# Performance work log

Measured on AMD Instinct MI355X. Metric: run time of the kernel, lower is better.

Reference implementation:

```python
import jax, jax.numpy as jnp
import numpy as np

N_P, N_W, F_IN = 512, 3584, 256
H1, O1 = 8, 32
H2, O2 = 8, 256
BATCH = 1024
NEG_SLOPE = 0.2


def _xavier(key, shape):
    fan_in, fan_out = shape[-2], shape[-1]
    lim = jnp.sqrt(6.0 / (fan_in + fan_out))
    return jax.random.uniform(key, shape, jnp.float32, -lim, lim)


def setup_inputs() -> dict:
    key = jax.random.key(0)
    ks = jax.random.split(key, 16)
    return {
        "input": jax.random.uniform(ks[0], (BATCH, N_W), jnp.float32),
        "pern_feature": jax.random.normal(ks[1], (N_P, F_IN), jnp.float32),
        "word_feature": jax.random.normal(ks[2], (N_W, F_IN), jnp.float32),
        "w1": _xavier(ks[3], (H1, F_IN, O1)),
        "a_src1": _xavier(ks[4], (H1, O1, 1)),
        "a_dst1": _xavier(ks[5], (H1, O1, 1)),
        "b1": jnp.zeros((O1,), jnp.float32),
        "w2": _xavier(ks[6], (H2, F_IN, O2)),
        "a_src2": _xavier(ks[7], (H2, F_IN, 1)),
        "a_dst2": _xavier(ks[8], (H2, F_IN, 1)),
        "b2": jnp.zeros((O2,), jnp.float32),
        "W_fc": _xavier(ks[9], (O2, 5)),
        "b_fc": jnp.zeros((5,), jnp.float32),
        "pern_adj": jax.random.randint(ks[10], (N_P, N_P), 0, 2, jnp.int32),
        "word_pern_adj": jax.random.randint(ks[11], (N_P + N_W, N_P + N_W), 0, 2, jnp.int32),
    }


def gat(h, adj, w, a_src, a_dst, bias):
    # h: [N, f_in], adj: [N, N] int, w: [H, f_in, f_out]
    h_prime = jnp.einsum('nf,hfo->hno', h, w)          # [H, N, O]
    t = jnp.tanh(h_prime)
    s_src = jnp.einsum('hno,hoi->hn', t, a_src)        # [H, N]
    s_dst = jnp.einsum('hno,hoi->hn', t, a_dst)        # [H, N]
    attn = s_src[:, :, None] + s_dst[:, None, :]       # [H, N, N]
    attn = jnp.where(attn >= 0, attn, NEG_SLOPE * attn)  # leaky_relu
    attn = jnp.where(adj[None, :, :] > 0, attn, -jnp.inf)
    attn = jax.nn.softmax(attn, axis=-1)
    out = jnp.einsum('hnm,hmo->hno', attn, h_prime)    # [H, N, O]
    return out + bias


def reference(input, pern_feature, word_feature, w1, a_src1, a_dst1, b1,
              w2, a_src2, a_dst2, b2, W_fc, b_fc, pern_adj, word_pern_adj):
    n_p = pern_feature.shape[0]
    # GAT 1 over personality graph
    h1 = gat(pern_feature, pern_adj, w1, a_src1, a_dst1, b1)       # [H1, n_p, O1]
    hiddn_pp = jnp.transpose(h1, (1, 0, 2)).reshape(n_p, -1)        # [n_p, H1*O1]
    hiddn_pp = jax.nn.elu(hiddn_pp)
    # dropout is identity in eval mode
    hiddn_wp = jnp.concatenate([word_feature, hiddn_pp], axis=0)    # [N, 256]
    h2 = gat(hiddn_wp, word_pern_adj, w2, a_src2, a_dst2, b2)       # [H2, N, O2]
    hiddn_wp2 = h2.mean(axis=0)                                     # [N, O2]
    hiddn_w = hiddn_wp2[:word_feature.shape[0], :]                  # [n_w, O2]
    x = (input @ hiddn_w) / input.sum(axis=1, keepdims=True)        # [B, O2]
    return x @ W_fc + b_fc                                          # [B, 5]
```

## Files before the change

### kernel.cpp

```cpp
#include <hip/hip_runtime.h>
#include <hip/hip_bf16.h>
#include <math.h>

#define NP 512
#define NW 3584
#define NT 4096
#define FIN 256
#define H1 8
#define O1 32
#define H2 8
#define O2 256
#define NEG 0.2f

typedef __attribute__((ext_vector_type(8))) short bf16x8;
typedef __attribute__((ext_vector_type(4))) float f32x4;
typedef unsigned long long u64;

__device__ __forceinline__ unsigned short f2bf(float f) {
    unsigned u = __float_as_uint(f);
    unsigned r = (u + 0x7FFF + ((u >> 16) & 1)) >> 16;
    return (unsigned short)r;
}

__device__ __forceinline__ float fast_tanh(float x) {
    float ex = __expf(2.0f * x);
    return 1.0f - 2.0f / (ex + 1.0f);
}

__device__ __forceinline__ float rfl(float x) {
    return __uint_as_float(__builtin_amdgcn_readfirstlane(__float_as_uint(x)));
}

__global__ void k_conv_word(const float* __restrict__ wf, unsigned short* __restrict__ abf) {
    int i = blockIdx.x * 256 + threadIdx.x;
    if (i < NW * FIN) abf[i] = f2bf(wf[i]);
}

__global__ __launch_bounds__(256) void k_gat1_hp(
    const float* __restrict__ pf, const float* __restrict__ w1,
    const float* __restrict__ a_src1, const float* __restrict__ a_dst1,
    float* __restrict__ hp1, float* __restrict__ ss1, float* __restrict__ sd1)
{
    __shared__ float feat[8][FIN];
    int t = threadIdx.x;
    int n0 = blockIdx.x * 8;
    for (int q = 0; q < 8; q++) {
        int idx = q * 256 + t;
        feat[idx >> 8][idx & 255] = pf[(n0 + (idx >> 8)) * FIN + (idx & 255)];
    }
    __syncthreads();
    int h = t >> 5, o = t & 31;
    float acc[8] = {0,0,0,0,0,0,0,0};
    const float* wcol = w1 + h * FIN * O1 + o;
    for (int f = 0; f < FIN; f++) {
        float w = wcol[f * O1];
        #pragma unroll
        for (int i = 0; i < 8; i++) acc[i] += feat[i][f] * w;
    }
    float as = a_src1[h * O1 + o];
    float ad = a_dst1[h * O1 + o];
    #pragma unroll
    for (int i = 0; i < 8; i++) {
        hp1[(n0 + i) * 256 + t] = acc[i];
        float th = tanhf(acc[i]);
        float vs = th * as, vd = th * ad;
        #pragma unroll
        for (int off = 1; off < 32; off <<= 1) {
            vs += __shfl_xor(vs, off);
            vd += __shfl_xor(vd, off);
        }
        if (o == 0) { ss1[h * NP + n0 + i] = vs; sd1[h * NP + n0 + i] = vd; }
    }
}

__global__ __launch_bounds__(256) void k_gat1_attn(
    const int* __restrict__ adj, const float* __restrict__ hp1,
    const float* __restrict__ ss1, const float* __restrict__ sd1,
    const float* __restrict__ b1, unsigned short* __restrict__ abf)
{
    __shared__ float p[2][H1][NP];
    __shared__ float den[2][H1];
    int t = threadIdx.x;
    int n0 = blockIdx.x * 2;
    for (int rr = 0; rr < 32; rr++) {
        int idx = rr * 256 + t;
        int i = idx >> 12, h = (idx >> 9) & 7, m = idx & 511;
        float a = adj[(n0 + i) * NP + m] > 0 ? 1.0f : 0.0f;
        float e = ss1[h * NP + n0 + i] + sd1[h * NP + m];
        e = fmaxf(e, NEG * e);
        p[i][h][m] = a * __expf(e);
    }
    __syncthreads();
    int w = t >> 6, l = t & 63;
    {
        int i = w & 1;
        #pragma unroll
        for (int hh = 0; hh < 4; hh++) {
            int h = (w >> 1) * 4 + hh;
            float s = 0;
            #pragma unroll
            for (int q = 0; q < 8; q++) s += p[i][h][l + 64 * q];
            #pragma unroll
            for (int off = 1; off < 64; off <<= 1) s += __shfl_xor(s, off);
            if (l == 0) den[i][h] = s;
        }
    }
    __syncthreads();
    int h = t >> 5, o = t & 31;
    float acc[2] = {0, 0};
    #pragma unroll 4
    for (int m = 0; m < NP; m++) {
        float v = hp1[m * 256 + t];
        acc[0] += p[0][h][m] * v;
        acc[1] += p[1][h][m] * v;
    }
    float bo = b1[o];
    #pragma unroll
    for (int i = 0; i < 2; i++) {
        float r = acc[i] / den[i][h] + bo;
        r = r > 0.f ? r : expm1f(r);
        abf[(NW + n0 + i) * FIN + t] = f2bf(r);
    }
}

__global__ void k_conv_w2(const float* __restrict__ w2, unsigned short* __restrict__ btbf) {
    int idx = blockIdx.x * 256 + threadIdx.x;
    int f = idx & 255, o = (idx >> 8) & 255, h = idx >> 16;
    btbf[idx] = f2bf(w2[(h * FIN + f) * O2 + o]);
}

__global__ __launch_bounds__(256) void k_pack_adj(const int* __restrict__ adj,
                                                  u64* __restrict__ packed) {
    int w = threadIdx.x >> 6, l = threadIdx.x & 63;
    int r = blockIdx.x * 4 + w;
    const int4* row = (const int4*)(adj + (size_t)r * NT);
    for (int c4 = 0; c4 < 16; c4++) {
        int4 x = row[c4 * 64 + l];
        u64 nib = (u64)((x.x != 0 ? 1 : 0) | (x.y != 0 ? 2 : 0) |
                        (x.z != 0 ? 4 : 0) | (x.w != 0 ? 8 : 0));
        u64 v = nib << (4 * (l & 15));
        v |= __shfl_xor(v, 1);
        v |= __shfl_xor(v, 2);
        v |= __shfl_xor(v, 4);
        v |= __shfl_xor(v, 8);
        if ((l & 15) == 0) packed[(size_t)r * 64 + c4 * 4 + (l >> 4)] = v;
    }
}

__global__ __launch_bounds__(256) void k_gemm_hp2(
    const unsigned short* __restrict__ abf, const unsigned short* __restrict__ btbf,
    const float* __restrict__ a_src2, const float* __restrict__ a_dst2,
    const float* __restrict__ W_fc, float* __restrict__ gpart)
{
    int bid = blockIdx.x;
    int h = bid >> 6;
    int rem = bid & 63;
    int mt = rem >> 1, nt = rem & 1;
    int w = threadIdx.x >> 6, l = threadIdx.x & 63;
    int m0 = mt * 128 + (w >> 1) * 64;
    int n0 = nt * 128 + (w & 1) * 64;
    int lr = l & 15, lq = l >> 4;
    const unsigned short* bbase = btbf + h * O2 * FIN;
    f32x4 acc[4][4];
    #pragma unroll
    for (int i = 0; i < 4; i++)
        #pragma unroll
        for (int j = 0; j < 4; j++) acc[i][j] = (f32x4){0.f, 0.f, 0.f, 0.f};
    for (int k = 0; k < FIN; k += 32) {
        bf16x8 a[4], b[4];
        int kc = k + lq * 8;
        #pragma unroll
        for (int i = 0; i < 4; i++)
            a[i] = *(const bf16x8*)(abf + (m0 + i * 16 + lr) * FIN + kc);
        #pragma unroll
        for (int j = 0; j < 4; j++)
            b[j] = *(const bf16x8*)(bbase + (n0 + j * 16 + lr) * FIN + kc);
        #pragma unroll
        for (int i = 0; i < 4; i++)
            #pragma unroll
            for (int j = 0; j < 4; j++)
                acc[i][j] = __builtin_amdgcn_mfma_f32_16x16x32_bf16(a[i], b[j], acc[i][j], 0, 0, 0);
    }
    int slice = nt * 2 + (w & 1);
    float as[4], ad[4], wfc[4][5];
    #pragma unroll
    for (int j = 0; j < 4; j++) {
        int col = n0 + j * 16 + lr;
        as[j] = a_src2[h * O2 + col];
        ad[j] = a_dst2[h * O2 + col];
        #pragma unroll
        for (int jj = 0; jj < 5; jj++) wfc[j][jj] = W_fc[col * 5 + jj];
    }
    float* base = gpart + ((size_t)h * 4 + slice) * NT * 8;
    #pragma unroll
    for (int i = 0; i < 4; i++) {
        #pragma unroll
        for (int r = 0; r < 4; r++) {
            float s[7] = {0,0,0,0,0,0,0};
            #pragma unroll
            for (int j = 0; j < 4; j++) {
                float x = acc[i][j][r];
                float th = fast_tanh(x);
                s[0] += th * as[j];
                s[1] += th * ad[j];
                #pragma unroll
                for (int jj = 0; jj < 5; jj++) s[2 + jj] += x * wfc[j][jj];
            }
            #pragma unroll
            for (int off = 1; off < 16; off <<= 1)
                #pragma unroll
                for (int q = 0; q < 7; q++) s[q] += __shfl_xor(s[q], off);
            if (lr == 0) {
                int m = m0 + i * 16 + lq * 4 + r;
                float* dst = base + (size_t)m * 8;
                #pragma unroll
                for (int q = 0; q < 7; q++) dst[q] = s[q];
            }
        }
    }
}

__global__ __launch_bounds__(256) void k_comb_hp2(
    const float* __restrict__ gpart,
    float* __restrict__ negss, float* __restrict__ Etab, float* __restrict__ Eptab,
    float* __restrict__ T)
{
    int idx = blockIdx.x * 256 + threadIdx.x;
    float s[7] = {0,0,0,0,0,0,0};
    #pragma unroll
    for (int sl = 0; sl < 4; sl++) {
        const float* p = gpart + (((size_t)(idx >> 12) * 4 + sl) * NT + (idx & (NT - 1))) * 8;
        #pragma unroll
        for (int q = 0; q < 7; q++) s[q] += p[q];
    }
    negss[idx] = -s[0];
    Etab[idx]  = __expf(s[0]);
    Eptab[idx] = __expf(NEG * s[0]);
    float4 t0 = {s[1], __expf(s[1]), __expf(NEG * s[1]), s[2]};
    float4 t1 = {s[3], s[4], s[5], s[6]};
    *(float4*)(T + (size_t)idx * 8)     = t0;
    *(float4*)(T + (size_t)idx * 8 + 4) = t1;
}

__global__ void k_cvec(const float* __restrict__ b2, const float* __restrict__ W_fc,
                       float* __restrict__ c) {
    int t = threadIdx.x;
    float v[5];
    #pragma unroll
    for (int j = 0; j < 5; j++) v[j] = b2[t] * W_fc[t * 5 + j];
    #pragma unroll
    for (int off = 1; off < 64; off <<= 1)
        #pragma unroll
        for (int j = 0; j < 5; j++) v[j] += __shfl_xor(v[j], off);
    __shared__ float red[4][5];
    int w = t >> 6, l = t & 63;
    if (l == 0) { for (int j = 0; j < 5; j++) red[w][j] = v[j]; }
    __syncthreads();
    if (t == 0)
        for (int j = 0; j < 5; j++) c[j] = red[0][j] + red[1][j] + red[2][j] + red[3][j];
}

__global__ __launch_bounds__(512) void k_gat2_attn(
    const u64* __restrict__ packed, const float* __restrict__ negss,
    const float* __restrict__ Etab, const float* __restrict__ Eptab,
    const float* __restrict__ T, float* __restrict__ part)
{
    __shared__ u64 pw[64 * 32];
    int t = threadIdx.x;
    int w = t >> 6, l = t & 63;
    int b = blockIdx.x;
    int nb = b % 56;
    int h  = (b / 56) & 7;
    int c  = b / 448;
    int rbase = nb * 64;
    #pragma unroll
    for (int u = 0; u < 4; u++) {
        int idx = u * 512 + t;
        int row = idx >> 5, q = idx & 31;
        pw[idx] = packed[(size_t)(rbase + row) * 64 + c * 32 + q];
    }
    __syncthreads();
    int n0 = rbase + w * 8;
    float ns[8], E[8], Ep[8];
    #pragma unroll
    for (int i = 0; i < 8; i++) {
        int r = h * NT + n0 + i;
        ns[i] = rfl(negss[r]);
        E[i]  = rfl(Etab[r]);
        Ep[i] = rfl(Eptab[r]);
    }
    float den[8] = {0,0,0,0,0,0,0,0};
    float num[8][5] = {{0}};
    const float* Th = T + ((size_t)h * NT + c * 2048) * 8;
    for (int q = 0; q < 32; q++) {
        const float* tp = Th + (size_t)(q * 64 + l) * 8;
        float4 t0 = *(const float4*)tp;
        float4 t1 = *(const float4*)(tp + 4);
        float sd = t0.x, F = t0.y, Fp = t0.z;
        float g0 = t0.w, g1 = t1.x, g2 = t1.y, g3 = t1.z, g4 = t1.w;
        #pragma unroll
        for (int i = 0; i < 8; i++) {
            u64 word = pw[(w * 8 + i) * 32 + q];
            float pa = F * E[i];
            float pb = Fp * Ep[i];
            float pp0 = (sd >= ns[i]) ? pa : pb;
            float pp = ((word >> l) & 1ull) ? pp0 : 0.0f;
            den[i] += pp;
            num[i][0] = fmaf(pp, g0, num[i][0]);
            num[i][1] = fmaf(pp, g1, num[i][1]);
            num[i][2] = fmaf(pp, g2, num[i][2]);
            num[i][3] = fmaf(pp, g3, num[i][3]);
            num[i][4] = fmaf(pp, g4, num[i][4]);
        }
    }
    #pragma unroll
    for (int i = 0; i < 8; i++) {
        float v[6];
        v[0] = den[i];
        #pragma unroll
        for (int j = 0; j < 5; j++) v[1 + j] = num[i][j];
        #pragma unroll
        for (int off = 1; off < 64; off <<= 1)
            #pragma unroll
            for (int k = 0; k < 6; k++) v[k] += __shfl_xor(v[k], off);
        if (l == 0) {
            float* dst = part + (((size_t)c * NW + n0 + i) * 8 + h) * 6;
            #pragma unroll
            for (int k = 0; k < 6; k++) dst[k] = v[k];
        }
    }
}

__global__ __launch_bounds__(256) void k_gat2_comb(const float* __restrict__ part,
                                                   float* __restrict__ hf) {
    int idx = blockIdx.x * 256 + threadIdx.x;
    int n = idx >> 3, h = idx & 7;
    float den = 0, num[5] = {0,0,0,0,0};
    #pragma unroll
    for (int cc = 0; cc < 2; cc++) {
        const float* p = part + (((size_t)cc * NW + n) * 8 + h) * 6;
        den += p[0];
        #pragma unroll
        for (int j = 0; j < 5; j++) num[j] += p[1 + j];
    }
    float inv = 1.0f / (den * 8.0f);
    float v[5];
    #pragma unroll
    for (int j = 0; j < 5; j++) v[j] = num[j] * inv;
    #pragma unroll
    for (int off = 1; off < 8; off <<= 1)
        #pragma unroll
        for (int j = 0; j < 5; j++) v[j] += __shfl_xor(v[j], off);
    if (h == 0) {
        #pragma unroll
        for (int j = 0; j < 5; j++) hf[n * 5 + j] = v[j];
    }
}

__global__ __launch_bounds__(256) void k_final(
    const float* __restrict__ input, const float* __restrict__ hf,
    const float* __restrict__ cvec, const float* __restrict__ b_fc,
    float* __restrict__ out)
{
    int b = blockIdx.x, t = threadIdx.x;
    const float4* row4 = (const float4*)(input + (size_t)b * NW);
    const float4* hf4 = (const float4*)hf;
    float s = 0.f, a[5] = {0.f, 0.f, 0.f, 0.f, 0.f};
    for (int idx = t; idx < NW / 4; idx += 256) {
        float4 x = row4[idx];
        float f[20];
        #pragma unroll
        for (int q = 0; q < 5; q++) *(float4*)(f + 4 * q) = hf4[idx * 5 + q];
        s += x.x + x.y + x.z + x.w;
        #pragma unroll
        for (int j = 0; j < 5; j++)
            a[j] += x.x * f[j] + x.y * f[5 + j] + x.z * f[10 + j] + x.w * f[15 + j];
    }
    #pragma unroll
    for (int off = 1; off < 64; off <<= 1) {
        s += __shfl_xor(s, off);
        #pragma unroll
        for (int j = 0; j < 5; j++) a[j] += __shfl_xor(a[j], off);
    }
    __shared__ float red[4][6];
    int w = t >> 6, l = t & 63;
    if (l == 0) { red[w][0] = s; for (int j = 0; j < 5; j++) red[w][j + 1] = a[j]; }
    __syncthreads();
    if (t < 5) {
        float st = red[0][0] + red[1][0] + red[2][0] + red[3][0];
        float aj = red[0][t + 1] + red[1][t + 1] + red[2][t + 1] + red[3][t + 1];
        out[b * 5 + t] = aj / st + cvec[t] + b_fc[t];
    }
}

extern "C" void kernel_launch(void* const* d_in, const int* in_sizes, int n_in,
                              void* d_out, int out_size, void* d_ws, size_t ws_size,
                              hipStream_t stream) {
    const float* input   = (const float*)d_in[0];
    const float* pf      = (const float*)d_in[1];
    const float* wf      = (const float*)d_in[2];
    const float* w1      = (const float*)d_in[3];
    const float* a_src1  = (const float*)d_in[4];
    const float* a_dst1  = (const float*)d_in[5];
    const float* b1      = (const float*)d_in[6];
    const float* w2      = (const float*)d_in[7];
    const float* a_src2  = (const float*)d_in[8];
    const float* a_dst2  = (const float*)d_in[9];
    const float* b2      = (const float*)d_in[10];
    const float* W_fc    = (const float*)d_in[11];
    const float* b_fc    = (const float*)d_in[12];
    const int* pern_adj  = (const int*)d_in[13];
    const int* wp_adj    = (const int*)d_in[14];
    float* out = (float*)d_out;

    char* ws = (char*)d_ws;
    unsigned short* abf    = (unsigned short*)(ws);
    unsigned short* btbf   = (unsigned short*)(ws + 2097152);
    float*          hp1    = (float*)(ws + 3145728);
    float*          ss1    = (float*)(ws + 3670016);
    float*          sd1    = (float*)(ws + 3686400);
    float*          negss  = (float*)(ws + 3702784);
    float*          Etab   = (float*)(ws + 3833856);
    float*          Eptab  = (float*)(ws + 3964928);
    float*          T      = (float*)(ws + 4096000);
    float*          hf     = (float*)(ws + 5144576);
    float*          cvec   = (float*)(ws + 5216256);
    u64*            packed = (u64*)(ws + 5216512);
    float*          gpart  = (float*)(ws + 7051520);
    float*          part   = (float*)(ws + 11245824);

    k_conv_word<<<3584, 256, 0, stream>>>(wf, abf);
    k_gat1_hp<<<64, 256, 0, stream>>>(pf, w1, a_src1, a_dst1, hp1, ss1, sd1);
    k_gat1_attn<<<256, 256, 0, stream>>>(pern_adj, hp1, ss1, sd1, b1, abf);
    k_conv_w2<<<2048, 256, 0, stream>>>(w2, btbf);
    k_pack_adj<<<896, 256, 0, stream>>>(wp_adj, packed);
    k_gemm_hp2<<<512, 256, 0, stream>>>(abf, btbf, a_src2, a_dst2, W_fc, gpart);
    k_comb_hp2<<<128, 256, 0, stream>>>(gpart, negss, Etab, Eptab, T);
    k_cvec<<<1, 256, 0, stream>>>(b2, W_fc, cvec);
    k_gat2_attn<<<896, 512, 0, stream>>>(packed, negss, Etab, Eptab, T, part);
    k_gat2_comb<<<112, 256, 0, stream>>>(part, hf);
    k_final<<<1024, 256, 0, stream>>>(input, hf, cvec, b_fc, out);
}
```

Baseline: 297.4 us.

## Merge prep kernels and use packed-math max trick in GAT2 attention loop

Five small preprocessing kernels (word conversion, GAT1 projection, w2 conversion, adjacency packing, bias vector) are merged into one launch with block-range dispatch. The GAT2 attention inner loop drops the sign comparison: since exp is monotonic, the leaky-relu branch equals the max of exp(s) and exp(0.2*s), so the branch becomes v_pk_mul plus fmax. The loop also uses packed FP32 FMAs and reads adjacency words directly from global via readfirstlane instead of staging them in LDS. This cuts launch overhead and ALU work, but relies on inline asm and uncached scalar-broadcast global loads.

New measurement: 314.0 us. 5.6% more time.

```diff
diff --git a/kernel.cpp b/kernel.cpp
--- a/kernel.cpp
+++ b/kernel.cpp
@@ -14,6 +14,7 @@
 
 typedef __attribute__((ext_vector_type(8))) short bf16x8;
 typedef __attribute__((ext_vector_type(4))) float f32x4;
+typedef __attribute__((ext_vector_type(2))) float v2f;
 typedef unsigned long long u64;
 
 __device__ __forceinline__ unsigned short f2bf(float f) {
@@ -27,49 +28,85 @@
     return 1.0f - 2.0f / (ex + 1.0f);
 }
 
-__device__ __forceinline__ float rfl(float x) {
-    return __uint_as_float(__builtin_amdgcn_readfirstlane(__float_as_uint(x)));
-}
-
-__global__ void k_conv_word(const float* __restrict__ wf, unsigned short* __restrict__ abf) {
-    int i = blockIdx.x * 256 + threadIdx.x;
-    if (i < NW * FIN) abf[i] = f2bf(wf[i]);
-}
-
-__global__ __launch_bounds__(256) void k_gat1_hp(
-    const float* __restrict__ pf, const float* __restrict__ w1,
-    const float* __restrict__ a_src1, const float* __restrict__ a_dst1,
-    float* __restrict__ hp1, float* __restrict__ ss1, float* __restrict__ sd1)
-{
-    __shared__ float feat[8][FIN];
+__global__ __launch_bounds__(256) void k_prep(
+    const float* __restrict__ wf, const float* __restrict__ pf,
+    const float* __restrict__ w1, const float* __restrict__ a_src1,
+    const float* __restrict__ a_dst1, const float* __restrict__ w2,
+    const float* __restrict__ b2, const float* __restrict__ W_fc,
+    const int* __restrict__ wp_adj,
+    unsigned short* __restrict__ abf, unsigned short* __restrict__ btbf,
+    float* __restrict__ hp1, float* __restrict__ ss1, float* __restrict__ sd1,
+    u64* __restrict__ packed, float* __restrict__ cvec)
+{
+    __shared__ float feat[2][FIN];
+    __shared__ float red[4][5];
+    int blk = blockIdx.x;
     int t = threadIdx.x;
-    int n0 = blockIdx.x * 8;
-    for (int q = 0; q < 8; q++) {
-        int idx = q * 256 + t;
-        feat[idx >> 8][idx & 255] = pf[(n0 + (idx >> 8)) * FIN + (idx & 255)];
-    }
-    __syncthreads();
-    int h = t >> 5, o = t & 31;
-    float acc[8] = {0,0,0,0,0,0,0,0};
-    const float* wcol = w1 + h * FIN * O1 + o;
-    for (int f = 0; f < FIN; f++) {
-        float w = wcol[f * O1];
-        #pragma unroll
-        for (int i = 0; i < 8; i++) acc[i] += feat[i][f] * w;
-    }
-    float as = a_src1[h * O1 + o];
-    float ad = a_dst1[h * O1 + o];
-    #pragma unroll
-    for (int i = 0; i < 8; i++) {
-        hp1[(n0 + i) * 256 + t] = acc[i];
-        float th = tanhf(acc[i]);
-        float vs = th * as, vd = th * ad;
-        #pragma unroll
-        for (int off = 1; off < 32; off <<= 1) {
-            vs += __shfl_xor(vs, off);
-            vd += __shfl_xor(vd, off);
-        }
-        if (o == 0) { ss1[h * NP + n0 + i] = vs; sd1[h * NP + n0 + i] = vd; }
+    if (blk < 3584) {
+        int i = blk * 256 + t;
+        abf[i] = f2bf(wf[i]);
+    } else if (blk < 3840) {
+        int n0 = (blk - 3584) * 2;
+        feat[0][t] = pf[n0 * FIN + t];
+        feat[1][t] = pf[(n0 + 1) * FIN + t];
+        __syncthreads();
+        int h = t >> 5, o = t & 31;
+        float acc0 = 0.f, acc1 = 0.f;
+        const float* wcol = w1 + h * FIN * O1 + o;
+        #pragma unroll 4
+        for (int f = 0; f < FIN; f++) {
+            float w = wcol[f * O1];
+            acc0 += feat[0][f] * w;
+            acc1 += feat[1][f] * w;
+        }
+        hp1[n0 * 256 + t] = acc0;
+        hp1[(n0 + 1) * 256 + t] = acc1;
+        float as = a_src1[h * O1 + o];
+        float ad = a_dst1[h * O1 + o];
+        float accs[2] = {acc0, acc1};
+        #pragma unroll
+        for (int i = 0; i < 2; i++) {
+            float th = tanhf(accs[i]);
+            float vs = th * as, vd = th * ad;
+            #pragma unroll
+            for (int off = 1; off < 32; off <<= 1) {
+                vs += __shfl_xor(vs, off);
+                vd += __shfl_xor(vd, off);
+            }
+            if (o == 0) { ss1[h * NP + n0 + i] = vs; sd1[h * NP + n0 + i] = vd; }
+        }
+    } else if (blk < 5888) {
+        int idx = (blk - 3840) * 256 + t;
+        int f = idx & 255, o = (idx >> 8) & 255, h = idx >> 16;
+        btbf[idx] = f2bf(w2[(h * FIN + f) * O2 + o]);
+    } else if (blk < 6784) {
+        int w = t >> 6, l = t & 63;
+        int r = (blk - 5888) * 4 + w;
+        const int4* row = (const int4*)(wp_adj + (size_t)r * NT);
+        for (int c4 = 0; c4 < 16; c4++) {
+            int4 x = row[c4 * 64 + l];
+            u64 nib = (u64)((x.x != 0 ? 1 : 0) | (x.y != 0 ? 2 : 0) |
+                            (x.z != 0 ? 4 : 0) | (x.w != 0 ? 8 : 0));
+            u64 v = nib << (4 * (l & 15));
+            v |= __shfl_xor(v, 1);
+            v |= __shfl_xor(v, 2);
+            v |= __shfl_xor(v, 4);
+            v |= __shfl_xor(v, 8);
+            if ((l & 15) == 0) packed[(size_t)r * 64 + c4 * 4 + (l >> 4)] = v;
+        }
+    } else {
+        float v[5];
+        #pragma unroll
+        for (int j = 0; j < 5; j++) v[j] = b2[t] * W_fc[t * 5 + j];
+        #pragma unroll
+        for (int off = 1; off < 64; off <<= 1)
+            #pragma unroll
+            for (int j = 0; j < 5; j++) v[j] += __shfl_xor(v[j], off);
+        int w = t >> 6, l = t & 63;
+        if (l == 0) { for (int j = 0; j < 5; j++) red[w][j] = v[j]; }
+        __syncthreads();
+        if (t == 0)
+            for (int j = 0; j < 5; j++) cvec[j] = red[0][j] + red[1][j] + red[2][j] + red[3][j];
     }
 }
 
@@ -123,30 +160,6 @@
     }
 }
 
-__global__ void k_conv_w2(const float* __restrict__ w2, unsigned short* __restrict__ btbf) {
-    int idx = blockIdx.x * 256 + threadIdx.x;
-    int f = idx & 255, o = (idx >> 8) & 255, h = idx >> 16;
-    btbf[idx] = f2bf(w2[(h * FIN + f) * O2 + o]);
-}
-
-__global__ __launch_bounds__(256) void k_pack_adj(const int* __restrict__ adj,
-                                                  u64* __restrict__ packed) {
-    int w = threadIdx.x >> 6, l = threadIdx.x & 63;
-    int r = blockIdx.x * 4 + w;
-    const int4* row = (const int4*)(adj + (size_t)r * NT);
-    for (int c4 = 0; c4 < 16; c4++) {
-        int4 x = row[c4 * 64 + l];
-        u64 nib = (u64)((x.x != 0 ? 1 : 0) | (x.y != 0 ? 2 : 0) |
-                        (x.z != 0 ? 4 : 0) | (x.w != 0 ? 8 : 0));
-        u64 v = nib << (4 * (l & 15));
-        v |= __shfl_xor(v, 1);
-        v |= __shfl_xor(v, 2);
-        v |= __shfl_xor(v, 4);
-        v |= __shfl_xor(v, 8);
-        if ((l & 15) == 0) packed[(size_t)r * 64 + c4 * 4 + (l >> 4)] = v;
-    }
-}
-
 __global__ __launch_bounds__(256) void k_gemm_hp2(
     const unsigned short* __restrict__ abf, const unsigned short* __restrict__ btbf,
     const float* __restrict__ a_src2, const float* __restrict__ a_dst2,
@@ -222,8 +235,7 @@
 
 __global__ __launch_bounds__(256) void k_comb_hp2(
     const float* __restrict__ gpart,
-    float* __restrict__ negss, float* __restrict__ Etab, float* __restrict__ Eptab,
-    float* __restrict__ T)
+    float* __restrict__ Etab, float* __restrict__ Eptab, float* __restrict__ T)
 {
     int idx = blockIdx.x * 256 + threadIdx.x;
     float s[7] = {0,0,0,0,0,0,0};
@@ -233,92 +245,72 @@
         #pragma unroll
         for (int q = 0; q < 7; q++) s[q] += p[q];
     }
-    negss[idx] = -s[0];
     Etab[idx]  = __expf(s[0]);
     Eptab[idx] = __expf(NEG * s[0]);
-    float4 t0 = {s[1], __expf(s[1]), __expf(NEG * s[1]), s[2]};
+    float4 t0 = {__expf(s[1]), __expf(NEG * s[1]), 1.0f, s[2]};
     float4 t1 = {s[3], s[4], s[5], s[6]};
     *(float4*)(T + (size_t)idx * 8)     = t0;
     *(float4*)(T + (size_t)idx * 8 + 4) = t1;
 }
 
-__global__ void k_cvec(const float* __restrict__ b2, const float* __restrict__ W_fc,
-                       float* __restrict__ c) {
-    int t = threadIdx.x;
-    float v[5];
-    #pragma unroll
-    for (int j = 0; j < 5; j++) v[j] = b2[t] * W_fc[t * 5 + j];
-    #pragma unroll
-    for (int off = 1; off < 64; off <<= 1)
-        #pragma unroll
-        for (int j = 0; j < 5; j++) v[j] += __shfl_xor(v[j], off);
-    __shared__ float red[4][5];
-    int w = t >> 6, l = t & 63;
-    if (l == 0) { for (int j = 0; j < 5; j++) red[w][j] = v[j]; }
-    __syncthreads();
-    if (t == 0)
-        for (int j = 0; j < 5; j++) c[j] = red[0][j] + red[1][j] + red[2][j] + red[3][j];
-}
-
 __global__ __launch_bounds__(512) void k_gat2_attn(
-    const u64* __restrict__ packed, const float* __restrict__ negss,
-    const float* __restrict__ Etab, const float* __restrict__ Eptab,
-    const float* __restrict__ T, float* __restrict__ part)
-{
-    __shared__ u64 pw[64 * 32];
+    const u64* __restrict__ packed, const float* __restrict__ Etab,
+    const float* __restrict__ Eptab, const float* __restrict__ T,
+    float* __restrict__ part)
+{
     int t = threadIdx.x;
     int w = t >> 6, l = t & 63;
     int b = blockIdx.x;
     int nb = b % 56;
     int h  = (b / 56) & 7;
     int c  = b / 448;
-    int rbase = nb * 64;
-    #pragma unroll
-    for (int u = 0; u < 4; u++) {
-        int idx = u * 512 + t;
-        int row = idx >> 5, q = idx & 31;
-        pw[idx] = packed[(size_t)(rbase + row) * 64 + c * 32 + q];
-    }
-    __syncthreads();
-    int n0 = rbase + w * 8;
-    float ns[8], E[8], Ep[8];
+    int n0 = nb * 64 + w * 8;
+    u64 epk[8];
     #pragma unroll
     for (int i = 0; i < 8; i++) {
         int r = h * NT + n0 + i;
-        ns[i] = rfl(negss[r]);
-        E[i]  = rfl(Etab[r]);
-        Ep[i] = rfl(Eptab[r]);
-    }
-    float den[8] = {0,0,0,0,0,0,0,0};
-    float num[8][5] = {{0}};
+        unsigned e  = __builtin_amdgcn_readfirstlane(__float_as_uint(Etab[r]));
+        unsigned ep = __builtin_amdgcn_readfirstlane(__float_as_uint(Eptab[r]));
+        epk[i] = ((u64)ep << 32) | e;
+    }
+    v2f accA[8], accB[8], accC[8];
+    #pragma unroll
+    for (int i = 0; i < 8; i++) {
+        accA[i] = (v2f){0.f, 0.f}; accB[i] = (v2f){0.f, 0.f}; accC[i] = (v2f){0.f, 0.f};
+    }
     const float* Th = T + ((size_t)h * NT + c * 2048) * 8;
+    const u64* prow = packed + c * 32;
     for (int q = 0; q < 32; q++) {
         const float* tp = Th + (size_t)(q * 64 + l) * 8;
-        float4 t0 = *(const float4*)tp;
-        float4 t1 = *(const float4*)(tp + 4);
-        float sd = t0.x, F = t0.y, Fp = t0.z;
-        float g0 = t0.w, g1 = t1.x, g2 = t1.y, g3 = t1.z, g4 = t1.w;
+        f32x4 t0 = *(const f32x4*)tp;
+        f32x4 t1 = *(const f32x4*)(tp + 4);
+        v2f ffp = {t0.x, t0.y};
+        v2f g01 = {t0.z, t0.w};
+        v2f g12 = {t1.x, t1.y};
+        v2f g34 = {t1.z, t1.w};
         #pragma unroll
         for (int i = 0; i < 8; i++) {
-            u64 word = pw[(w * 8 + i) * 32 + q];
-            float pa = F * E[i];
-            float pb = Fp * Ep[i];
-            float pp0 = (sd >= ns[i]) ? pa : pb;
-            float pp = ((word >> l) & 1ull) ? pp0 : 0.0f;
-            den[i] += pp;
-            num[i][0] = fmaf(pp, g0, num[i][0]);
-            num[i][1] = fmaf(pp, g1, num[i][1]);
-            num[i][2] = fmaf(pp, g2, num[i][2]);
-            num[i][3] = fmaf(pp, g3, num[i][3]);
-            num[i][4] = fmaf(pp, g4, num[i][4]);
+            u64 wv = prow[(size_t)(n0 + i) * 64 + q];
+            unsigned wlo = __builtin_amdgcn_readfirstlane((unsigned)wv);
+            unsigned whi = __builtin_amdgcn_readfirstlane((unsigned)(wv >> 32));
+            u64 word = ((u64)whi << 32) | wlo;
+            v2f pab;
+            asm("v_pk_mul_f32 %0, %1, %2" : "=v"(pab) : "v"(ffp), "s"(epk[i]));
+            float pp0 = fmaxf(pab.x, pab.y);
+            float pp;
+            asm("v_cndmask_b32 %0, 0, %1, %2" : "=v"(pp) : "v"(pp0), "s"(word));
+            v2f ppv; ppv.x = pp; ppv.y = pp;
+            asm("v_pk_fma_f32 %0, %1, %2, %0" : "+v"(accA[i]) : "v"(ppv), "v"(g01));
+            asm("v_pk_fma_f32 %0, %1, %2, %0" : "+v"(accB[i]) : "v"(ppv), "v"(g12));
+            asm("v_pk_fma_f32 %0, %1, %2, %0" : "+v"(accC[i]) : "v"(ppv), "v"(g34));
         }
     }
     #pragma unroll
     for (int i = 0; i < 8; i++) {
         float v[6];
-        v[0] = den[i];
-        #pragma unroll
-        for (int j = 0; j < 5; j++) v[1 + j] = num[i][j];
+        v[0] = accA[i].x; v[1] = accA[i].y;
+        v[2] = accB[i].x; v[3] = accB[i].y;
+        v[4] = accC[i].x; v[5] = accC[i].y;
         #pragma unroll
         for (int off = 1; off < 64; off <<= 1)
             #pragma unroll
@@ -419,7 +411,6 @@
     float*          hp1    = (float*)(ws + 3145728);
     float*          ss1    = (float*)(ws + 3670016);
     float*          sd1    = (float*)(ws + 3686400);
-    float*          negss  = (float*)(ws + 3702784);
     float*          Etab   = (float*)(ws + 3833856);
     float*          Eptab  = (float*)(ws + 3964928);
     float*          T      = (float*)(ws + 4096000);
@@ -429,15 +420,12 @@
     float*          gpart  = (float*)(ws + 7051520);
     float*          part   = (float*)(ws + 11245824);
 
-    k_conv_word<<<3584, 256, 0, stream>>>(wf, abf);
-    k_gat1_hp<<<64, 256, 0, stream>>>(pf, w1, a_src1, a_dst1, hp1, ss1, sd1);
+    k_prep<<<6785, 256, 0, stream>>>(wf, pf, w1, a_src1, a_dst1, w2, b2, W_fc,
+                                     wp_adj, abf, btbf, hp1, ss1, sd1, packed, cvec);
     k_gat1_attn<<<256, 256, 0, stream>>>(pern_adj, hp1, ss1, sd1, b1, abf);
-    k_conv_w2<<<2048, 256, 0, stream>>>(w2, btbf);
-    k_pack_adj<<<896, 256, 0, stream>>>(wp_adj, packed);
     k_gemm_hp2<<<512, 256, 0, stream>>>(abf, btbf, a_src2, a_dst2, W_fc, gpart);
-    k_comb_hp2<<<128, 256, 0, stream>>>(gpart, negss, Etab, Eptab, T);
-    k_cvec<<<1, 256, 0, stream>>>(b2, W_fc, cvec);
-    k_gat2_attn<<<896, 512, 0, stream>>>(packed, negss, Etab, Eptab, T, part);
+    k_comb_hp2<<<128, 256, 0, stream>>>(gpart, Etab, Eptab, T);
+    k_gat2_attn<<<896, 512, 0, stream>>>(packed, Etab, Eptab, T, part);
     k_gat2_comb<<<112, 256, 0, stream>>>(part, hf);
     k_final<<<1024, 256, 0, stream>>>(input, hf, cvec, b_fc, out);
 }
```
